# Kernel tuning notes

Measured on AMD Instinct MI355X. Metric: run time of the kernel, lower is better.

The kernel has to match this reference:

```python
import jax, jax.numpy as jnp
import numpy as np

B, L, D, NLAYERS, MAX_NODES, DEG = 32, 512, 768, 3, 128, 8


def _build_graph():
    rng = np.random.default_rng(0)
    per = rng.integers(-32, 33, size=B // 2)
    sizes = np.concatenate([96 + per, 96 - per]).astype(np.int64)  # sum = 96*B = 3072, each in [64,128]
    N = int(sizes.sum())
    offs = np.concatenate([[0], np.cumsum(sizes)])
    batch = np.repeat(np.arange(B), sizes).astype(np.int64)
    pad_idx = np.zeros((B, MAX_NODES), np.int64)
    pad_mask = np.zeros((B, MAX_NODES), bool)
    src, dst = [], []
    for b in range(B):
        n = int(sizes[b])
        pad_idx[b, :n] = np.arange(offs[b], offs[b] + n)
        pad_mask[b, :n] = True
        src.append(rng.integers(offs[b], offs[b] + n, n * DEG))
        dst.append(rng.integers(offs[b], offs[b] + n, n * DEG))
    return N, batch, pad_idx, pad_mask, np.concatenate(src), np.concatenate(dst)


def setup_inputs() -> dict:
    N, batch, pad_idx, pad_mask, esrc, edst = _build_graph()
    key = jax.random.key(0)
    ks = jax.random.split(key, 8)
    s = 1.0 / np.sqrt(D)
    return {
        "x": jax.random.normal(ks[0], (N, D), jnp.float32),
        "text": jax.random.normal(ks[1], (B, L, D), jnp.float32),
        "batch_ent1_d_mask": jnp.ones((B, 1), jnp.float32),
        "batch_ent1_g_mask": jnp.ones((B, 1), jnp.float32),
        "gnn_ws": jax.random.normal(ks[2], (NLAYERS, D, D), jnp.float32) * s,
        "gnn_wn": jax.random.normal(ks[3], (NLAYERS, D, D), jnp.float32) * s,
        "gnn_b": jnp.zeros((NLAYERS, D), jnp.float32),
        "atom_w": jax.random.normal(ks[4], (D, D), jnp.float32) * s,
        "atom_b": jnp.zeros((D,), jnp.float32),
        "rand_emb": jax.random.normal(ks[5], (1, D), jnp.float32),
        "batch": jnp.asarray(batch),
        "pad_idx": jnp.asarray(pad_idx),
        "pad_mask": jnp.asarray(pad_mask),
        "edge_src": jnp.asarray(esrc),
        "edge_dst": jnp.asarray(edst),
    }


def reference(x, text, batch_ent1_d_mask, batch_ent1_g_mask, gnn_ws, gnn_wn, gnn_b,
              atom_w, atom_b, rand_emb, batch, pad_idx, pad_mask, edge_src, edge_dst):
    N = x.shape[0]
    E = edge_src.shape[0]
    maskf = pad_mask.astype(x.dtype)            # [B, M]
    n_per = maskf.sum(axis=1)                   # [B] num real nodes per graph
    # edge-neighbor mean counts (constants w.r.t. x)
    cnt = jax.ops.segment_sum(jnp.ones((E,), x.dtype), edge_dst, num_segments=N)
    inv_cnt = 1.0 / jnp.maximum(cnt, 1.0)
    cms = []
    for i in range(NLAYERS):
        # MoleGraphConv stand-in: mean neighbor aggregation + self transform
        msg = jax.ops.segment_sum(x[edge_src], edge_dst, num_segments=N) * inv_cnt[:, None]
        x = jax.nn.relu(x @ gnn_ws[i] + msg @ gnn_wn[i] + gnn_b[i])
        # ragged gather into padded [B, M, D]
        xp = x[pad_idx] * maskf[..., None]
        # graph -> text cross attention (softmax over text tokens; no mask needed)
        g2t = jax.nn.softmax(jnp.einsum('bmd,bld->bml', xp, text), axis=-1)
        g2t_out = jnp.einsum('bml,bld->bmd', g2t, text)            # [B, M, D]
        # text -> graph cross attention (mask padded nodes)
        t2g_logits = jnp.einsum('bld,bmd->blm', text, xp)
        t2g_logits = jnp.where(pad_mask[:, None, :], t2g_logits, jnp.float32(-1e9))
        t2g = jax.nn.softmax(t2g_logits, axis=-1)
        t2g_out = jnp.einsum('blm,bmd->bld', t2g, xp)              # [B, L, D]
        # mean over concatenated rows [n_i + L] per graph (pool_type=2)
        pooled = ((g2t_out * maskf[..., None]).sum(axis=1) + t2g_out.sum(axis=1)) \
                 / (n_per + jnp.float32(L))[:, None]
        cms.append(pooled)
    out_cms = jnp.mean(jnp.stack(cms, axis=1), axis=1)              # mean over layers
    out_t = text[:, 0, :]
    # scatter-mean of final node features per graph
    gsum = jax.ops.segment_sum(x, batch, num_segments=B)
    gcnt = jax.ops.segment_sum(jnp.ones((N,), x.dtype), batch, num_segments=B)
    xg = gsum / jnp.maximum(gcnt, 1.0)[:, None]
    # dropout is a no-op in eval mode
    out_g = jnp.tanh(xg @ atom_w + atom_b)
    z = rand_emb[0]
    dg = batch_ent1_d_mask * batch_ent1_g_mask
    return jnp.concatenate([
        out_t * batch_ent1_d_mask + (1 - batch_ent1_d_mask) * z,
        out_g * batch_ent1_g_mask + (1 - batch_ent1_g_mask) * z,
        out_cms * dg + (1 - dg) * z,
    ], axis=-1)
```

## Files before the change

kernel.cpp:

```cpp
#include <hip/hip_runtime.h>

#define D 768
#define B 32
#define L 512
#define M 128
#define NNODES 3072
#define NEDGES 24576

using bf16x8 = __attribute__((ext_vector_type(8))) short;
using f32x4  = __attribute__((ext_vector_type(4))) float;

__device__ __forceinline__ float bf2f(unsigned short u) {
  union { unsigned int i; float f; } v; v.i = ((unsigned int)u) << 16; return v.f;
}
__device__ __forceinline__ unsigned short f2bf(float f) {
  union { float f; unsigned int i; } v; v.f = f;
  unsigned int x = v.i;
  return (unsigned short)((x + 0x7FFFu + ((x >> 16) & 1u)) >> 16);
}
__device__ __forceinline__ float ldf(const void* p, size_t i, int f32) {
  return f32 ? ((const float*)p)[i] : bf2f(((const unsigned short*)p)[i]);
}
__device__ __forceinline__ int ldi(const void* p, size_t i, int w64) {
  return w64 ? (int)((const long long*)p)[i] : ((const int*)p)[i];
}
__device__ __forceinline__ f32x4 mfma16(bf16x8 a, bf16x8 b, f32x4 c) {
  return __builtin_amdgcn_mfma_f32_16x16x32_bf16(a, b, c, 0, 0, 0);
}
__device__ __forceinline__ void gl_lds(const unsigned short* gsrc, unsigned short* lbase,
                                       int lane) {
  __builtin_amdgcn_global_load_lds(
      (const __attribute__((address_space(1))) unsigned int*)(gsrc + lane * 8),
      (__attribute__((address_space(3))) unsigned int*)lbase, 16, 0, 0);
}

__device__ __forceinline__ float pk_read(const unsigned short* P, int p, int l, int d) {
  return bf2f(P[(((size_t)(p * 24 + (d >> 5))) << 9) + ((((d & 31) >> 3) << 4) + l) * 8 + (d & 7)]);
}

__device__ __forceinline__ void fma8(float* acc, float w, uint4 v) {
  unsigned xs[4] = {v.x, v.y, v.z, v.w};
#pragma unroll
  for (int j = 0; j < 4; ++j) {
    acc[2 * j]     += w * bf2f((unsigned short)(xs[j] & 0xFFFFu));
    acc[2 * j + 1] += w * bf2f((unsigned short)(xs[j] >> 16));
  }
}

__device__ __forceinline__ void acc12(float* a, const uint2* u) {
#pragma unroll
  for (int j = 0; j < 3; ++j) {
    a[j * 4 + 0] += bf2f((unsigned short)(u[j].x & 0xFFFFu));
    a[j * 4 + 1] += bf2f((unsigned short)(u[j].x >> 16));
    a[j * 4 + 2] += bf2f((unsigned short)(u[j].y & 0xFFFFu));
    a[j * 4 + 3] += bf2f((unsigned short)(u[j].y >> 16));
  }
}


__device__ void d_pack_in(const void* src, unsigned short* rows, unsigned short* dst,
                          int p, int tid, int f) {
  unsigned short* pb = dst + (size_t)p * 12288;
  uint4 qv[6];
  if (f) {
    float4 v0[6], v1[6];
#pragma unroll
    for (int j = 0; j < 6; ++j) {
      int odx = j * 256 + tid;
      int kk = odx >> 6, lanep = odx & 63;
      size_t sbase = (size_t)(p * 16 + (lanep & 15)) * 768 + kk * 32 + ((lanep >> 4) << 3);
      const float* sp = (const float*)src + sbase;
      v0[j] = *(const float4*)sp;
      v1[j] = *(const float4*)(sp + 4);
    }
#pragma unroll
    for (int j = 0; j < 6; ++j) {
      union { unsigned short v[8]; uint4 q; } u;
      u.v[0] = f2bf(v0[j].x); u.v[1] = f2bf(v0[j].y); u.v[2] = f2bf(v0[j].z); u.v[3] = f2bf(v0[j].w);
      u.v[4] = f2bf(v1[j].x); u.v[5] = f2bf(v1[j].y); u.v[6] = f2bf(v1[j].z); u.v[7] = f2bf(v1[j].w);
      qv[j] = u.q;
    }
  } else {
#pragma unroll
    for (int j = 0; j < 6; ++j) {
      int odx = j * 256 + tid;
      int kk = odx >> 6, lanep = odx & 63;
      size_t sbase = (size_t)(p * 16 + (lanep & 15)) * 768 + kk * 32 + ((lanep >> 4) << 3);
      qv[j] = *(const uint4*)((const unsigned short*)src + sbase);
    }
  }
#pragma unroll
  for (int j = 0; j < 6; ++j) {
    int odx = j * 256 + tid;
    int kk = odx >> 6, lanep = odx & 63;
    size_t sbase = (size_t)(p * 16 + (lanep & 15)) * 768 + kk * 32 + ((lanep >> 4) << 3);
    if (rows) *(uint4*)&rows[sbase] = qv[j];
    *(uint4*)&pb[(size_t)odx * 8] = qv[j];
  }
}

__device__ void d_pack(const unsigned short* src, unsigned short* dst,
                       int p, int tid) {
  unsigned short* pb = dst + (size_t)p * 12288;
  uint4 qv[6];
#pragma unroll
  for (int j = 0; j < 6; ++j) {
    int odx = j * 256 + tid;
    int kk = odx >> 6, lanep = odx & 63;
    size_t sbase = (size_t)(p * 16 + (lanep & 15)) * 768 + kk * 32 + ((lanep >> 4) << 3);
    qv[j] = *(const uint4*)(src + sbase);
  }
#pragma unroll
  for (int j = 0; j < 6; ++j) {
    *(uint4*)&pb[(size_t)(j * 256 + tid) * 8] = qv[j];
  }
}

__device__ void d_wpack(const void* Ws, const void* Wn, const void* Aw, int f,
                        unsigned short* WsPk, unsigned short* WnPk, unsigned short* AwPk,
                        int r0, int tid) {
  int z = r0 / 288, rem = r0 % 288;
  int nblk = rem % 12, kk = rem / 12;
  const void* src; unsigned short* dst; size_t zoff;
  if (z < 3)      { src = Ws; zoff = (size_t)z * D * D;       dst = WsPk + zoff; }
  else if (z < 6) { src = Wn; zoff = (size_t)(z - 3) * D * D; dst = WnPk + zoff; }
  else            { src = Aw; zoff = 0;                       dst = AwPk; }
  int pl = tid >> 6, lane = tid & 63;
  int pG = nblk * 4 + pl;
  int k0 = kk * 32 + ((lane >> 4) << 3);
  int n  = nblk * 64 + pl * 16 + (lane & 15);
  union { unsigned short v[8]; uint4 q; } u;
  if (f) {
    const float* sp = (const float*)src + zoff + (size_t)k0 * D + n;
#pragma unroll
    for (int e = 0; e < 8; ++e) u.v[e] = f2bf(sp[(size_t)e * D]);
  } else {
    const unsigned short* sp = (const unsigned short*)src + zoff + (size_t)k0 * D + n;
#pragma unroll
    for (int e = 0; e < 8; ++e) u.v[e] = sp[(size_t)e * D];
  }
  *(uint4*)&dst[(((size_t)(pG * 24 + kk)) << 9) + lane * 8] = u.q;
}

__device__ void d_count(const void* edst, const void* batch, int w,
                        int* cnt, int* gcnt, int i) {
  if (i < NEDGES) atomicAdd(&cnt[ldi(edst, i, w)], 1);
  if (i < NNODES) atomicAdd(&gcnt[ldi(batch, i, w)], 1);
}

__device__ void d_msg(const unsigned short* x, const int* cnt, const int* rowstart,
                      const int* csr, unsigned short* Mpk, int p, int tid) {
  int w = tid >> 6, lane = tid & 63;
  unsigned short* pb = Mpk + (size_t)p * 12288;
#pragma unroll
  for (int i = 0; i < 4; i += 2) {
    int rA = w * 4 + i, rB = rA + 1;
    int nA = p * 16 + rA, nB = p * 16 + rB;
    int degA = cnt[nA], baseA = rowstart[nA];
    int degB = cnt[nB], baseB = rowstart[nB];
    float aA[12], aB[12];
#pragma unroll
    for (int j = 0; j < 12; ++j) { aA[j] = 0.f; aB[j] = 0.f; }
    int dmax = degA > degB ? degA : degB;
    for (int e = 0; e < dmax; ++e) {
      uint2 uA[3], uB[3];
      if (e < degA) {
        const uint2* xr = (const uint2*)(x + (size_t)csr[baseA + e] * D);
        uA[0] = xr[lane]; uA[1] = xr[lane + 64]; uA[2] = xr[lane + 128];
      }
      if (e < degB) {
        const uint2* xr = (const uint2*)(x + (size_t)csr[baseB + e] * D);
        uB[0] = xr[lane]; uB[1] = xr[lane + 64]; uB[2] = xr[lane + 128];
      }
      if (e < degA) acc12(aA, uA);
      if (e < degB) acc12(aB, uB);
    }
    float invA = 1.0f / (float)(degA > 1 ? degA : 1);
    float invB = 1.0f / (float)(degB > 1 ? degB : 1);
#pragma unroll
    for (int j = 0; j < 3; ++j) {
      int d0 = (lane + j * 64) * 4;
      int kk = d0 >> 5, q = (d0 >> 3) & 3, e0 = d0 & 7;
      uint2 wA, wB;
      wA.x = (unsigned int)f2bf(aA[j * 4 + 0] * invA)
           | ((unsigned int)f2bf(aA[j * 4 + 1] * invA) << 16);
      wA.y = (unsigned int)f2bf(aA[j * 4 + 2] * invA)
           | ((unsigned int)f2bf(aA[j * 4 + 3] * invA) << 16);
      wB.x = (unsigned int)f2bf(aB[j * 4 + 0] * invB)
           | ((unsigned int)f2bf(aB[j * 4 + 1] * invB) << 16);
      wB.y = (unsigned int)f2bf(aB[j * 4 + 2] * invB)
           | ((unsigned int)f2bf(aB[j * 4 + 3] * invB) << 16);
      *(uint2*)&pb[kk * 512 + (q * 16 + rA) * 8 + e0] = wA;
      *(uint2*)&pb[kk * 512 + (q * 16 + rB) * 8 + e0] = wB;
    }
  }
}

__device__ void d_gemm(const unsigned short* Xpk, const unsigned short* Mpk,
                       const unsigned short* WsPk, const unsigned short* WnPk,
                       const void* bias, size_t bias_off, int f,
                       unsigned short* Y, int bx, int by, int tid, char* smem) {
  unsigned short* lds = (unsigned short*)smem;
  int wave = tid >> 6, lane = tid & 63;
  int q = lane >> 4, t = lane & 15;
  int wm = wave >> 1, wn = wave & 1;
  int pa = bx * 4, pb = by * 4;
  f32x4 acc[2][2];
#pragma unroll
  for (int mi = 0; mi < 2; ++mi)
#pragma unroll
    for (int ni = 0; ni < 2; ++ni)
      acc[mi][ni] = (f32x4){0.f, 0.f, 0.f, 0.f};
  int c0 = wave * 2;
  int pan0 = (wave < 2) ? (pa + c0) : (pb + c0 - 4);
  auto issue = [&](int r) {
    unsigned short* dbuf = &lds[(r % 3) * 8192 + c0 * 512];
#pragma unroll
    for (int st = 0; st < 2; ++st) {
      int s = r * 2 + st;
      int h = (s >= 24) ? 1 : 0;
      const unsigned short* P = (wave < 2) ? (h ? Mpk : Xpk) : (h ? WnPk : WsPk);
      int kk = s - h * 24;
      gl_lds(P + (((size_t)(pan0 * 24 + kk)) << 9), dbuf + st * 4096, lane);
      gl_lds(P + (((size_t)((pan0 + 1) * 24 + kk)) << 9), dbuf + st * 4096 + 512, lane);
    }
  };
  issue(0);
  issue(1);
  for (int r = 0; r < 24; ++r) {
    if (r < 23) asm volatile("s_waitcnt vmcnt(4)" ::: "memory");
    else        asm volatile("s_waitcnt vmcnt(0)" ::: "memory");
    __builtin_amdgcn_s_barrier();
    asm volatile("" ::: "memory");
    if (r < 22) issue(r + 2);
    const unsigned short* bb = &lds[(r % 3) * 8192];
#pragma unroll
    for (int st = 0; st < 2; ++st) {
      const unsigned short* bs = bb + st * 4096;
      bf16x8 a0 = *(const bf16x8*)&bs[(wm * 2 + 0) * 512 + lane * 8];
      bf16x8 a1 = *(const bf16x8*)&bs[(wm * 2 + 1) * 512 + lane * 8];
      bf16x8 b0 = *(const bf16x8*)&bs[(4 + wn * 2 + 0) * 512 + lane * 8];
      bf16x8 b1 = *(const bf16x8*)&bs[(4 + wn * 2 + 1) * 512 + lane * 8];
      acc[0][0] = mfma16(a0, b0, acc[0][0]);
      acc[0][1] = mfma16(a0, b1, acc[0][1]);
      acc[1][0] = mfma16(a1, b0, acc[1][0]);
      acc[1][1] = mfma16(a1, b1, acc[1][1]);
    }
    asm volatile("" ::: "memory");
  }
#pragma unroll
  for (int ni = 0; ni < 2; ++ni) {
    int col = by * 64 + wn * 32 + ni * 16 + t;
    float bv = ldf(bias, bias_off + col, f);
#pragma unroll
    for (int mi = 0; mi < 2; ++mi) {
#pragma unroll
      for (int r = 0; r < 4; ++r) {
        int row = bx * 64 + wm * 32 + mi * 16 + q * 4 + r;
        float v = acc[mi][ni][r] + bv;
        Y[(size_t)row * D + col] = f2bf(v > 0.f ? v : 0.f);
      }
    }
  }
}

__device__ void d_xp(const unsigned short* Xn, const void* pidx, int w64,
                     const int* gcnt, unsigned short* xp, unsigned short* XpPk,
                     float* xgacc, int p, int tid, char* smem) {
  unsigned short* rows = (unsigned short*)smem;
  int r = tid >> 4, c16 = tid & 15;
  int bm = p * 16 + r;
  int b = bm >> 7, m = bm & 127;
  int nb = gcnt[b];
  uint4* dl = (uint4*)&rows[r * 776];
  uint4 v[6];
  if (m < nb) {
    const uint4* srcr = (const uint4*)(Xn + (size_t)ldi(pidx, bm, w64) * D);
#pragma unroll
    for (int j = 0; j < 6; ++j) v[j] = srcr[c16 + j * 16];
  } else {
    uint4 z = {0u, 0u, 0u, 0u};
#pragma unroll
    for (int j = 0; j < 6; ++j) v[j] = z;
  }
#pragma unroll
  for (int j = 0; j < 6; ++j) dl[c16 + j * 16] = v[j];
  __syncthreads();
#pragma unroll
  for (int j = 0; j < 6; ++j) {
    int idx = j * 256 + tid;
    int rr = idx / 96, cc = idx % 96;
    uint4 vv = *(const uint4*)&rows[rr * 776 + cc * 8];
    *(uint4*)&xp[(size_t)(p * 16 + rr) * D + cc * 8] = vv;
  }
  unsigned short* pb = XpPk + (size_t)p * 12288;
#pragma unroll
  for (int j = 0; j < 6; ++j) {
    int odx = j * 256 + tid;
    int kk = odx >> 6, lanep = odx & 63;
    int rr = lanep & 15, cg = lanep >> 4;
    int cc = kk * 4 + cg;
    uint4 vv = *(const uint4*)&rows[rr * 776 + cc * 8];
    *(uint4*)&pb[odx * 8] = vv;
  }
  if (xgacc) {
    int bb = p >> 3;
#pragma unroll
    for (int j = 0; j < 3; ++j) {
      int d = j * 256 + tid;
      float s = 0.f;
#pragma unroll
      for (int rr = 0; rr < 16; ++rr) s += bf2f(rows[rr * 776 + d]);
      atomicAdd(&xgacc[(size_t)bb * D + d], s);
    }
  }
}

__device__ void d_scores(const unsigned short* XpPk, const unsigned short* Tpk,
                         float* S, int bx, int by, int bz, int tid, char* smem) {
  unsigned short* lds = (unsigned short*)smem;
  int wave = tid >> 6, lane = tid & 63;
  int q = lane >> 4, t = lane & 15;
  int wm = wave >> 1, wn = wave & 1;
  int pa = bz * 8 + bx * 4;
  int pb = bz * 32 + by * 4;
  f32x4 acc[2][2];
#pragma unroll
  for (int mi = 0; mi < 2; ++mi)
#pragma unroll
    for (int ni = 0; ni < 2; ++ni)
      acc[mi][ni] = (f32x4){0.f, 0.f, 0.f, 0.f};
  int c0 = wave * 2;
  const unsigned short* P = (wave < 2) ? XpPk : Tpk;
  int pan0 = (wave < 2) ? (pa + c0) : (pb + c0 - 4);
  auto issue = [&](int r) {
    unsigned short* dbuf = &lds[(r % 3) * 8192 + c0 * 512];
#pragma unroll
    for (int st = 0; st < 2; ++st) {
      int kk = r * 2 + st;
      gl_lds(P + (((size_t)(pan0 * 24 + kk)) << 9), dbuf + st * 4096, lane);
      gl_lds(P + (((size_t)((pan0 + 1) * 24 + kk)) << 9), dbuf + st * 4096 + 512, lane);
    }
  };
  issue(0);
  issue(1);
  for (int r = 0; r < 12; ++r) {
    if (r < 11) asm volatile("s_waitcnt vmcnt(4)" ::: "memory");
    else        asm volatile("s_waitcnt vmcnt(0)" ::: "memory");
    __builtin_amdgcn_s_barrier();
    asm volatile("" ::: "memory");
    if (r < 10) issue(r + 2);
    const unsigned short* bb = &lds[(r % 3) * 8192];
#pragma unroll
    for (int st = 0; st < 2; ++st) {
      const unsigned short* bs = bb + st * 4096;
      bf16x8 a0 = *(const bf16x8*)&bs[(wm * 2 + 0) * 512 + lane * 8];
      bf16x8 a1 = *(const bf16x8*)&bs[(wm * 2 + 1) * 512 + lane * 8];
      bf16x8 b0 = *(const bf16x8*)&bs[(4 + wn * 2 + 0) * 512 + lane * 8];
      bf16x8 b1 = *(const bf16x8*)&bs[(4 + wn * 2 + 1) * 512 + lane * 8];
      acc[0][0] = mfma16(a0, b0, acc[0][0]);
      acc[0][1] = mfma16(a0, b1, acc[0][1]);
      acc[1][0] = mfma16(a1, b0, acc[1][0]);
      acc[1][1] = mfma16(a1, b1, acc[1][1]);
    }
    asm volatile("" ::: "memory");
  }
  float* Sb = S + (size_t)bz * M * L;
#pragma unroll
  for (int ni = 0; ni < 2; ++ni) {
    int col = by * 64 + wn * 32 + ni * 16 + t;
#pragma unroll
    for (int mi = 0; mi < 2; ++mi) {
#pragma unroll
      for (int r = 0; r < 4; ++r) {
        int row = bx * 64 + wm * 32 + mi * 16 + q * 4 + r;
        Sb[(size_t)row * L + col] = acc[mi][ni][r];
      }
    }
  }
}

__device__ void d_stats(const float* S, const int* gcnt, float* rmax, float* rsum,
                        float* cmaxv, float* csumv, int bid, int tid, char* smem) {
  if (bid < B * M) {
    float* red = (float*)smem;
    int lane = tid & 63, wv = tid >> 6;
    const float* r = S + (size_t)bid * L;
    float s0 = r[tid], s1 = r[tid + 256];
    float m = fmaxf(s0, s1);
#pragma unroll
    for (int o = 32; o > 0; o >>= 1) m = fmaxf(m, __shfl_down(m, o));
    if (lane == 0) red[wv] = m;
    __syncthreads();
    float bm = fmaxf(fmaxf(red[0], red[1]), fmaxf(red[2], red[3]));
    __syncthreads();
    float e = __expf(s0 - bm) + __expf(s1 - bm);
#pragma unroll
    for (int o = 32; o > 0; o >>= 1) e += __shfl_down(e, o);
    if (lane == 0) red[wv] = e;
    __syncthreads();
    if (tid == 0) { rmax[bid] = bm; rsum[bid] = red[0] + red[1] + red[2] + red[3]; }
  } else {
    float (*pm)[64] = (float(*)[64])smem;
    float (*ps)[64] = (float(*)[64])(smem + 1024);
    int cid = bid - B * M;
    int b = cid >> 3, ly = cid & 7;
    int w = tid >> 6, lane = tid & 63;
    int l = ly * 64 + lane;
    int nb = gcnt[b];
    const float* Sb = S + (size_t)b * M * L;
    int m0 = w * 32, m1 = min(m0 + 32, nb);
    float cm = -1e30f, cs = 0.f;
    for (int m = m0; m < m1; ++m) {
      float s = Sb[(size_t)m * L + l];
      if (s > cm) { cs = cs * __expf(cm - s) + 1.f; cm = s; }
      else cs += __expf(s - cm);
    }
    pm[w][lane] = cm; ps[w][lane] = cs;
    __syncthreads();
    if (w == 0) {
      float CM = -1e30f;
#pragma unroll
      for (int j = 0; j < 4; ++j) CM = fmaxf(CM, pm[j][lane]);
      float CS = 0.f;
#pragma unroll
      for (int j = 0; j < 4; ++j) CS += ps[j][lane] * __expf(pm[j][lane] - CM);
      cmaxv[b * L + l] = CM; csumv[b * L + l] = CS;
    }
  }
}

__device__ void d_cross(const float* S, const float* rmax, const float* rsum,
                        const float* cmaxv, const float* csumv, const int* gcnt,
                        float* wv, float* t2gcol, int bid, int tid, char* smem) {
  if (bid < 256) {
    float* rm = (float*)smem;
    float* ri = (float*)(smem + 512);
    float (*pw)[64] = (float(*)[64])(smem + 1024);
    int b = bid >> 3, ly = bid & 7;
    int w = tid >> 6, lane = tid & 63;
    if (tid < M) { rm[tid] = rmax[b * M + tid]; ri[tid] = 1.f / rsum[b * M + tid]; }
    __syncthreads();
    int l = ly * 64 + lane;
    int nb = gcnt[b];
    const float* Sb = S + (size_t)b * M * L;
    int m0 = w * 32, m1 = min(m0 + 32, nb);
    float wp = 0.f;
    for (int m = m0; m < m1; ++m)
      wp += __expf(Sb[(size_t)m * L + l] - rm[m]) * ri[m];
    pw[w][lane] = wp;
    __syncthreads();
    if (w == 0)
      wv[b * L + l] = pw[0][lane] + pw[1][lane] + pw[2][lane] + pw[3][lane];
  } else {
    float* red = (float*)smem;
    int bm = bid - 256;
    int b = bm >> 7, m = bm & 127;
    int lane = tid & 63, w = tid >> 6;
    int nb = gcnt[b];
    float acc = 0.f;
    if (m < nb) {
      const float* r = S + (size_t)bm * L;
      const float* cm = cmaxv + b * L;
      const float* cs = csumv + b * L;
      acc = __expf(r[tid] - cm[tid]) / cs[tid]
          + __expf(r[tid + 256] - cm[tid + 256]) / cs[tid + 256];
    }
#pragma unroll
    for (int o = 32; o > 0; o >>= 1) acc += __shfl_down(acc, o);
    if (lane == 0) red[w] = acc;
    __syncthreads();
    if (tid == 0) t2gcol[bm] = red[0] + red[1] + red[2] + red[3];
  }
}

__device__ void d_pooled(const float* wv, const float* t2gcol, const unsigned short* Tpk,
                         const unsigned short* xp, const int* gcnt, float* pooled,
                         int bid, int tid, char* smem) {
  float* lred = (float*)smem;
  float* wbuf = (float*)(smem + 3072);
  int b = bid / 10, seg = bid - b * 10;
  int chunk = tid % 96, half = tid / 96;
  int d = chunk * 8;
  float acc[8];
#pragma unroll
  for (int j = 0; j < 8; ++j) acc[j] = 0.f;
  if (tid < 64) {
    wbuf[tid] = (seg < 8) ? wv[b * L + seg * 64 + tid]
                          : t2gcol[b * M + (seg - 8) * 64 + tid];
  }
  __syncthreads();
  if (half < 2) {
    if (seg < 8) {
      int pbase = b * 32 + seg * 4;
      size_t cbase = ((size_t)(d >> 5)) << 9;
      int coff = ((d & 31) >> 3) << 4;
      for (int i = 0; i < 32; ++i) {
        int l = half * 32 + i;
        const unsigned short* src =
            Tpk + (((size_t)((pbase + (l >> 4)) * 24)) << 9) + cbase +
            (size_t)(coff + (l & 15)) * 8;
        fma8(acc, wbuf[l], *(const uint4*)src);
      }
    } else {
      const unsigned short* Xb = xp + (size_t)b * M * D + d;
      int m0 = (seg - 8) * 64;
      for (int i = 0; i < 32; ++i) {
        int mm = half * 32 + i;
        fma8(acc, wbuf[mm], *(const uint4*)&Xb[(size_t)(m0 + mm) * D]);
      }
    }
  }
  if (half == 1) {
#pragma unroll
    for (int j = 0; j < 8; ++j) lred[chunk * 8 + j] = acc[j];
  }
  __syncthreads();
  if (half == 0) {
    float inv = 1.f / ((float)gcnt[b] + 512.f);
#pragma unroll
    for (int j = 0; j < 8; ++j)
      atomicAdd(&pooled[(size_t)b * D + d + j], (acc[j] + lred[chunk * 8 + j]) * inv);
  }
}

__device__ void d_atom(const float* xgacc, const int* gcnt, const unsigned short* AwPk,
                       float* gpre, int bid, int tid) {
  int w = tid >> 6, lane = tid & 63;
  int q = lane >> 4, t = lane & 15;
  int nbase = bid * 64 + w * 16;
  int pb = nbase >> 4;
  int n0 = gcnt[t], n1 = gcnt[16 + t];
  float inv0 = 1.f / (float)(n0 > 1 ? n0 : 1);
  float inv1 = 1.f / (float)(n1 > 1 ? n1 : 1);
  f32x4 acc[2];
  acc[0] = (f32x4){0.f, 0.f, 0.f, 0.f};
  acc[1] = (f32x4){0.f, 0.f, 0.f, 0.f};
  for (int kk = 0; kk < 24; ++kk) {
    const float* s0 = xgacc + (size_t)t * D + kk * 32 + q * 8;
    const float* s1 = xgacc + (size_t)(16 + t) * D + kk * 32 + q * 8;
    union { unsigned short v[8]; bf16x8 f; } a0, a1;
#pragma unroll
    for (int j = 0; j < 8; ++j) { a0.v[j] = f2bf(s0[j] * inv0); a1.v[j] = f2bf(s1[j] * inv1); }
    bf16x8 bv = *(const bf16x8*)(AwPk + (((size_t)(pb * 24 + kk)) << 9) + (lane << 3));
    acc[0] = mfma16(a0.f, bv, acc[0]);
    acc[1] = mfma16(a1.f, bv, acc[1]);
  }
#pragma unroll
  for (int mi = 0; mi < 2; ++mi)
#pragma unroll
    for (int r = 0; r < 4; ++r) {
      int row = mi * 16 + q * 4 + r;
      gpre[(size_t)row * D + nbase + t] = acc[mi][r];
    }
}


__global__ void k_init(int* cnt, int* cursor, int* gcnt, float* pooled, float* xgacc,
                       const unsigned short* __restrict__ t,
                       const unsigned int* __restrict__ e, int* __restrict__ flags) {
  int i = blockIdx.x * 256 + threadIdx.x;
  if (i < NNODES) { cnt[i] = 0; cursor[i] = 0; }
  if (i < B) gcnt[i] = 0;
  if (i < B * D) { pooled[i] = 0.f; xgacc[i] = 0.f; }
  if (blockIdx.x == 0) {
    __shared__ int r0[256];
    __shared__ unsigned r1[256];
    int tid = threadIdx.x;
    int bad = 0;
    for (int j = tid; j < 8192; j += 256) {
      unsigned short u = t[2 * j];
      unsigned ex = (u >> 7) & 0xFF;
      if (ex >= 0xC0) bad = 1;
    }
    unsigned o = 0;
    for (int j = tid; j < NEDGES / 2; j += 256) o |= e[2 * j + 1];
    r0[tid] = bad; r1[tid] = o;
    __syncthreads();
    for (int s = 128; s > 0; s >>= 1) {
      if (tid < s) { r0[tid] |= r0[tid + s]; r1[tid] |= r1[tid + s]; }
      __syncthreads();
    }
    if (tid == 0) { flags[0] = r0[0]; flags[1] = (r1[0] == 0) ? 1 : 0; }
  }
}

__global__ __launch_bounds__(256) void k_setup2(
    const void* x_in, unsigned short* x0, unsigned short* PkA,
    const void* text, unsigned short* Tpk,
    const void* Ws, const void* Wn, const void* Aw,
    unsigned short* WsPk, unsigned short* WnPk, unsigned short* AwPk,
    const void* edst, const void* batch, int* cnt, int* gcnt,
    const int* __restrict__ flags) {
  int bid = blockIdx.x, tid = threadIdx.x;
  if (bid < 1216) {
    int f = flags[0];
    if (bid < NNODES / 16) d_pack_in(x_in, x0, PkA, bid, tid, f);
    else d_pack_in(text, nullptr, Tpk, bid - NNODES / 16, tid, f);
  } else if (bid < 3232) {
    d_wpack(Ws, Wn, Aw, flags[0], WsPk, WnPk, AwPk, bid - 1216, tid);
  } else {
    d_count(edst, batch, flags[1], cnt, gcnt, (bid - 3232) * 256 + tid);
  }
}

__global__ void k_scan(const int* __restrict__ cnt, int* __restrict__ rowstart) {
  __shared__ int a[NNODES], b[NNODES];
  int tid = threadIdx.x;
  for (int i = tid; i < NNODES; i += 1024) a[i] = cnt[i];
  __syncthreads();
  int* s = a; int* d = b;
  for (int off = 1; off < NNODES; off <<= 1) {
    for (int i = tid; i < NNODES; i += 1024)
      d[i] = s[i] + (i >= off ? s[i - off] : 0);
    __syncthreads();
    int* t = s; s = d; d = t;
  }
  for (int i = tid; i < NNODES; i += 1024) rowstart[i + 1] = s[i];
  if (tid == 0) rowstart[0] = 0;
}

__global__ void k_scatter(const void* __restrict__ esrc, const void* __restrict__ edst,
                          const int* __restrict__ flags, const int* __restrict__ rowstart,
                          int* __restrict__ cursor, int* __restrict__ csr) {
  int w = flags[1];
  int i = blockIdx.x * 256 + threadIdx.x;
  if (i < NEDGES) {
    int dd = ldi(edst, i, w);
    int pos = atomicAdd(&cursor[dd], 1);
    csr[rowstart[dd] + pos] = ldi(esrc, i, w);
  }
}

__global__ __launch_bounds__(256) void k_msgp(
    const unsigned short* x, const int* cnt, const int* rowstart, const int* csr,
    unsigned short* Mpk) {
  d_msg(x, cnt, rowstart, csr, Mpk, blockIdx.x, threadIdx.x);
}

__device__ __forceinline__ void gemm_map(int g, int& bx, int& by) {
  int gs = (g % 8) * 72 + g / 8;
  bx = gs / 12; by = gs % 12;
}
__device__ __forceinline__ void sc_map(int g, int& bx, int& by, int& bz) {
  int gs = (g % 8) * 64 + g / 8;
  bx = gs & 1; by = (gs >> 1) & 7; bz = gs >> 4;
}

__global__ __launch_bounds__(256) void k_gemm(
    const unsigned short* Apk, const unsigned short* Mpk,
    const unsigned short* WsPk, const unsigned short* WnPk,
    const void* bias, unsigned long bias_off, const int* flags, unsigned short* Y) {
  extern __shared__ char smem[];
  int bx, by; gemm_map(blockIdx.x, bx, by);
  d_gemm(Apk, Mpk, WsPk, WnPk, bias, bias_off, flags[0], Y, bx, by,
         threadIdx.x, smem);
}

__global__ __launch_bounds__(256) void k_postg(
    const unsigned short* Y, unsigned short* Npk, int packN,
    const void* pidx, const int* flags, const int* gcnt,
    unsigned short* xp, unsigned short* XpPk, float* xgacc) {
  extern __shared__ char smem[];
  int bid = blockIdx.x, tid = threadIdx.x;
  if (bid < 256) d_xp(Y, pidx, flags[1], gcnt, xp, XpPk, xgacc, bid, tid, smem);
  else d_pack(Y, Npk, bid - 256, tid);
}

__global__ __launch_bounds__(256) void k_scmsg(
    const unsigned short* XpPk, const unsigned short* Tpk, float* S,
    int msgN, const unsigned short* x, const int* cnt, const int* rowstart,
    const int* csr, unsigned short* Mpk) {
  extern __shared__ char smem[];
  int bid = blockIdx.x, tid = threadIdx.x;
  if (bid < msgN) d_msg(x, cnt, rowstart, csr, Mpk, bid, tid);
  else {
    int bx, by, bz; sc_map(bid - msgN, bx, by, bz);
    d_scores(XpPk, Tpk, S, bx, by, bz, tid, smem);
  }
}

__global__ __launch_bounds__(256) void k_stgemm(
    const float* S, const int* gcnt, float* rmax, float* rsum, float* cmaxv, float* csumv,
    int gemmN, const unsigned short* Apk, const unsigned short* Mpk,
    const unsigned short* WsPk, const unsigned short* WnPk,
    const void* bias, unsigned long bias_off, const int* flags, unsigned short* Y) {
  extern __shared__ char smem[];
  int bid = blockIdx.x, tid = threadIdx.x;
  if (bid < gemmN) {
    int bx, by; gemm_map(bid, bx, by);
    d_gemm(Apk, Mpk, WsPk, WnPk, bias, bias_off, flags[0], Y, bx, by, tid, smem);
  } else d_stats(S, gcnt, rmax, rsum, cmaxv, csumv, bid - gemmN, tid, smem);
}

__global__ __launch_bounds__(256) void k_crpostg(
    const float* S, const float* rmax, const float* rsum, const float* cmaxv,
    const float* csumv, const int* gcnt, float* wv, float* t2gcol,
    int packN, int xpN, const unsigned short* Y, unsigned short* Npk,
    const void* pidx, const int* flags, unsigned short* xp, unsigned short* XpPk,
    float* xgacc) {
  extern __shared__ char smem[];
  int bid = blockIdx.x, tid = threadIdx.x;
  if (bid < packN) { d_pack(Y, Npk, bid, tid); return; }
  int r = bid - packN;
  if (r < xpN) { d_xp(Y, pidx, flags[1], gcnt, xp, XpPk, xgacc, r, tid, smem); return; }
  d_cross(S, rmax, rsum, cmaxv, csumv, gcnt, wv, t2gcol, r - xpN, tid, smem);
}

__global__ __launch_bounds__(256) void k_plscmsg(
    const float* wv, const float* t2gcol, const unsigned short* Tpk,
    const unsigned short* xpL, const int* gcnt, float* pooled,
    int scN, const unsigned short* XpPk, float* S,
    int msgN, const unsigned short* x, const int* cnt, const int* rowstart,
    const int* csr, unsigned short* Mpk,
    int atomN, const float* xgacc, const unsigned short* AwPk, float* gpre) {
  extern __shared__ char smem[];
  int bid = blockIdx.x, tid = threadIdx.x;
  if (bid < msgN) { d_msg(x, cnt, rowstart, csr, Mpk, bid, tid); return; }
  int r = bid - msgN;
  if (r < scN) {
    int bx, by, bz; sc_map(r, bx, by, bz);
    d_scores(XpPk, Tpk, S, bx, by, bz, tid, smem); return;
  }
  r -= scN;
  if (r < 320) { d_pooled(wv, t2gcol, Tpk, xpL, gcnt, pooled, r, tid, smem); return; }
  d_atom(xgacc, gcnt, AwPk, gpre, r - 320, tid);
}

__global__ __launch_bounds__(256) void k_final(
    const unsigned short* __restrict__ Tpk, const float* __restrict__ gpre,
    const float* __restrict__ pooled, const void* __restrict__ ab,
    const void* __restrict__ dmask, const void* __restrict__ gmask,
    const void* __restrict__ remb, const int* __restrict__ flags,
    void* __restrict__ out) {
  int f = flags[0];
  int b = blockIdx.x, tid = threadIdx.x;
  float dm = ldf(dmask, b, f);
  float gm = ldf(gmask, b, f);
  float dg = dm * gm;
  size_t base = (size_t)b * 2304;
#pragma unroll
  for (int j = 0; j < 3; ++j) {
    int d = tid + j * 256;
    float z = ldf(remb, d, f);
    float tv = pk_read(Tpk, b * 32, 0, d);
    float o0 = tv * dm + (1.f - dm) * z;
    float gv = tanhf(gpre[(size_t)b * D + d] + ldf(ab, d, f));
    float o1 = gv * gm + (1.f - gm) * z;
    float p = pooled[(size_t)b * D + d] * (1.f / 3.f);
    float o2 = p * dg + (1.f - dg) * z;
    if (f) {
      float* of = (float*)out;
      of[base + d] = o0; of[base + 768 + d] = o1; of[base + 1536 + d] = o2;
    } else {
      unsigned short* ob = (unsigned short*)out;
      ob[base + d] = f2bf(o0); ob[base + 768 + d] = f2bf(o1); ob[base + 1536 + d] = f2bf(o2);
    }
  }
}

extern "C" void kernel_launch(void* const* d_in, const int* in_sizes, int n_in,
                              void* d_out, int out_size, void* d_ws, size_t ws_size,
                              hipStream_t stream) {
  const void* x_in  = d_in[0];
  const void* text  = d_in[1];
  const void* dmask = d_in[2];
  const void* gmask = d_in[3];
  const void* gws   = d_in[4];
  const void* gwn   = d_in[5];
  const void* gb    = d_in[6];
  const void* aw    = d_in[7];
  const void* ab    = d_in[8];
  const void* remb  = d_in[9];
  const void* batch = d_in[10];
  const void* pidx  = d_in[11];
  const void* esrc  = d_in[13];
  const void* edst  = d_in[14];

  char* wsp = (char*)d_ws;
  size_t off = 0;
  auto carve = [&](size_t bytes) -> void* {
    void* p = wsp + off;
    off += (bytes + 255) & ~(size_t)255;
    return p;
  };
  int* flags = (int*)carve(2 * 4);
  unsigned short* x0    = (unsigned short*)carve((size_t)NNODES * D * 2);
  unsigned short* xA    = (unsigned short*)carve((size_t)NNODES * D * 2);
  unsigned short* xB    = (unsigned short*)carve((size_t)NNODES * D * 2);
  unsigned short* PkA   = (unsigned short*)carve((size_t)NNODES * D * 2);
  unsigned short* PkB   = (unsigned short*)carve((size_t)NNODES * D * 2);
  unsigned short* Mpk   = (unsigned short*)carve((size_t)NNODES * D * 2);
  unsigned short* Tpk   = (unsigned short*)carve((size_t)B * L * D * 2);
  unsigned short* WsPk  = (unsigned short*)carve((size_t)3 * D * D * 2);
  unsigned short* WnPk  = (unsigned short*)carve((size_t)3 * D * D * 2);
  unsigned short* AwPk  = (unsigned short*)carve((size_t)D * D * 2);
  unsigned short* xpA   = (unsigned short*)carve((size_t)B * M * D * 2);
  unsigned short* xpB   = (unsigned short*)carve((size_t)B * M * D * 2);
  unsigned short* XpPkA = (unsigned short*)carve((size_t)B * M * D * 2);
  unsigned short* XpPkB = (unsigned short*)carve((size_t)B * M * D * 2);
  float* xgacc   = (float*)carve((size_t)B * D * 4);
  float* gpre    = (float*)carve((size_t)B * D * 4);
  float* S       = (float*)carve((size_t)B * M * L * 4);
  float* rmax    = (float*)carve((size_t)B * M * 4);
  float* rsum    = (float*)carve((size_t)B * M * 4);
  float* wv      = (float*)carve((size_t)B * L * 4);
  float* cmaxv   = (float*)carve((size_t)B * L * 4);
  float* csumv   = (float*)carve((size_t)B * L * 4);
  float* t2gcol  = (float*)carve((size_t)B * M * 4);
  float* pooled  = (float*)carve((size_t)B * D * 4);
  int* cnt      = (int*)carve((size_t)NNODES * 4);
  int* rowstart = (int*)carve((size_t)(NNODES + 1) * 4);
  int* cursor   = (int*)carve((size_t)NNODES * 4);
  int* gcnt     = (int*)carve((size_t)B * 4);
  int* csr      = (int*)carve((size_t)NEDGES * 4);

  const size_t DD = (size_t)D * D;

  k_init<<<96, 256, 0, stream>>>(cnt, cursor, gcnt, pooled, xgacc,
                                 (const unsigned short*)text, (const unsigned int*)edst, flags);
  k_setup2<<<3328, 256, 0, stream>>>(x_in, x0, PkA, text, Tpk, gws, gwn, aw,
                                     WsPk, WnPk, AwPk, edst, batch, cnt, gcnt, flags);
  k_scan<<<1, 1024, 0, stream>>>(cnt, rowstart);
  k_scatter<<<96, 256, 0, stream>>>(esrc, edst, flags, rowstart, cursor, csr);

  k_msgp<<<192, 256, 0, stream>>>(x0, cnt, rowstart, csr, Mpk);
  k_gemm<<<576, 256, 49152, stream>>>(PkA, Mpk, WsPk, WnPk, gb, 0, flags, xA);
  k_postg<<<448, 256, 24832, stream>>>(xA, PkB, 192, pidx, flags, gcnt, xpA, XpPkA, nullptr);
  k_scmsg<<<704, 256, 49152, stream>>>(XpPkA, Tpk, S, 192, xA, cnt, rowstart, csr, Mpk);
  k_stgemm<<<4928, 256, 49152, stream>>>(S, gcnt, rmax, rsum, cmaxv, csumv,
                                         576, PkB, Mpk, WsPk + DD, WnPk + DD, gb, D, flags, xB);
  k_crpostg<<<4800, 256, 24832, stream>>>(S, rmax, rsum, cmaxv, csumv, gcnt, wv, t2gcol,
                                          192, 256, xB, PkA, pidx, flags, xpB, XpPkB, nullptr);
  k_plscmsg<<<1024, 256, 49152, stream>>>(wv, t2gcol, Tpk, xpA, gcnt, pooled,
                                          512, XpPkB, S, 192, xB, cnt, rowstart, csr, Mpk,
                                          0, nullptr, nullptr, nullptr);
  k_stgemm<<<4928, 256, 49152, stream>>>(S, gcnt, rmax, rsum, cmaxv, csumv,
                                         576, PkA, Mpk, WsPk + 2 * DD, WnPk + 2 * DD,
                                         gb, 2 * D, flags, xA);
  k_crpostg<<<4608, 256, 24832, stream>>>(S, rmax, rsum, cmaxv, csumv, gcnt, wv, t2gcol,
                                          0, 256, xA, nullptr, pidx, flags, xpA, XpPkA, xgacc);
  k_plscmsg<<<832, 256, 49152, stream>>>(wv, t2gcol, Tpk, xpB, gcnt, pooled,
                                         512, XpPkA, S, 0, nullptr, nullptr, nullptr,
                                         nullptr, nullptr, 0, nullptr, nullptr, nullptr);
  k_stgemm<<<4352, 256, 2048, stream>>>(S, gcnt, rmax, rsum, cmaxv, csumv,
                                        0, nullptr, nullptr, nullptr, nullptr,
                                        nullptr, 0, flags, nullptr);
  k_crpostg<<<4352, 256, 2048, stream>>>(S, rmax, rsum, cmaxv, csumv, gcnt, wv, t2gcol,
                                         0, 0, nullptr, nullptr, pidx, flags,
                                         nullptr, nullptr, nullptr);
  k_plscmsg<<<332, 256, 4096, stream>>>(wv, t2gcol, Tpk, xpA, gcnt, pooled,
                                        0, nullptr, nullptr, 0, nullptr, nullptr, nullptr,
                                        nullptr, nullptr, 12, xgacc, AwPk, gpre);
  k_final<<<32, 256, 0, stream>>>(Tpk, gpre, pooled, ab, dmask, gmask, remb, flags, d_out);
}
```

Before: 434.0 us.

## Deepen GEMM LDS pipeline, shrink LDS, reorder fused block roles, aggregate gcnt atomics

The GEMM and scores mainloops switch from three 2-step LDS stages to a four-slot ring of single k-steps, three of them in flight, which shrinks LDS per block from 48KB to 32KB so more blocks can be resident. The fused kernels reorder block-index dispatch so the long stats/cross/pooled/scores work is placed in the low block indices and the short pack/msg work in the high ones. The node-count atomics are aggregated per wave through a ballot run-length, and the pack routines interleave load and store instead of batching loads. The risk is less latency hiding per barrier, since each barrier now covers half as much MFMA work.

```diff
diff --git a/kernel.cpp b/kernel.cpp
--- a/kernel.cpp
+++ b/kernel.cpp
@@ -61,58 +61,39 @@
 __device__ void d_pack_in(const void* src, unsigned short* rows, unsigned short* dst,
                           int p, int tid, int f) {
   unsigned short* pb = dst + (size_t)p * 12288;
-  uint4 qv[6];
-  if (f) {
-    float4 v0[6], v1[6];
-#pragma unroll
-    for (int j = 0; j < 6; ++j) {
-      int odx = j * 256 + tid;
-      int kk = odx >> 6, lanep = odx & 63;
-      size_t sbase = (size_t)(p * 16 + (lanep & 15)) * 768 + kk * 32 + ((lanep >> 4) << 3);
-      const float* sp = (const float*)src + sbase;
-      v0[j] = *(const float4*)sp;
-      v1[j] = *(const float4*)(sp + 4);
-    }
-#pragma unroll
-    for (int j = 0; j < 6; ++j) {
-      union { unsigned short v[8]; uint4 q; } u;
-      u.v[0] = f2bf(v0[j].x); u.v[1] = f2bf(v0[j].y); u.v[2] = f2bf(v0[j].z); u.v[3] = f2bf(v0[j].w);
-      u.v[4] = f2bf(v1[j].x); u.v[5] = f2bf(v1[j].y); u.v[6] = f2bf(v1[j].z); u.v[7] = f2bf(v1[j].w);
-      qv[j] = u.q;
-    }
-  } else {
-#pragma unroll
-    for (int j = 0; j < 6; ++j) {
-      int odx = j * 256 + tid;
-      int kk = odx >> 6, lanep = odx & 63;
-      size_t sbase = (size_t)(p * 16 + (lanep & 15)) * 768 + kk * 32 + ((lanep >> 4) << 3);
-      qv[j] = *(const uint4*)((const unsigned short*)src + sbase);
-    }
-  }
 #pragma unroll
   for (int j = 0; j < 6; ++j) {
     int odx = j * 256 + tid;
     int kk = odx >> 6, lanep = odx & 63;
-    size_t sbase = (size_t)(p * 16 + (lanep & 15)) * 768 + kk * 32 + ((lanep >> 4) << 3);
-    if (rows) *(uint4*)&rows[sbase] = qv[j];
-    *(uint4*)&pb[(size_t)odx * 8] = qv[j];
+    int q = lanep >> 4, r16 = lanep & 15;
+    int row = p * 16 + r16, col0 = kk * 32 + q * 8;
+    size_t sbase = (size_t)row * 768 + col0;
+    union { unsigned short v[8]; uint4 qv; } u;
+    if (f) {
+      const float* sp = (const float*)src + sbase;
+      float4 v0 = *(const float4*)sp;
+      float4 v1 = *(const float4*)(sp + 4);
+      u.v[0] = f2bf(v0.x); u.v[1] = f2bf(v0.y); u.v[2] = f2bf(v0.z); u.v[3] = f2bf(v0.w);
+      u.v[4] = f2bf(v1.x); u.v[5] = f2bf(v1.y); u.v[6] = f2bf(v1.z); u.v[7] = f2bf(v1.w);
+    } else {
+      u.qv = *(const uint4*)((const unsigned short*)src + sbase);
+    }
+    if (rows) *(uint4*)&rows[sbase] = u.qv;
+    *(uint4*)&pb[(size_t)odx * 8] = u.qv;
   }
 }
 
 __device__ void d_pack(const unsigned short* src, unsigned short* dst,
                        int p, int tid) {
   unsigned short* pb = dst + (size_t)p * 12288;
-  uint4 qv[6];
 #pragma unroll
   for (int j = 0; j < 6; ++j) {
     int odx = j * 256 + tid;
     int kk = odx >> 6, lanep = odx & 63;
-    size_t sbase = (size_t)(p * 16 + (lanep & 15)) * 768 + kk * 32 + ((lanep >> 4) << 3);
-    qv[j] = *(const uint4*)(src + sbase);
-  }
-#pragma unroll
-  for (int j = 0; j < 6; ++j) {
-    *(uint4*)&pb[(size_t)(j * 256 + tid) * 8] = qv[j];
+    int q = lanep >> 4, r16 = lanep & 15;
+    size_t sbase = (size_t)(p * 16 + r16) * 768 + kk * 32 + q * 8;
+    uint4 qv = *(const uint4*)(src + sbase);
+    *(uint4*)&pb[(size_t)odx * 8] = qv;
   }
 }
 
@@ -145,7 +126,18 @@
 __device__ void d_count(const void* edst, const void* batch, int w,
                         int* cnt, int* gcnt, int i) {
   if (i < NEDGES) atomicAdd(&cnt[ldi(edst, i, w)], 1);
-  if (i < NNODES) atomicAdd(&gcnt[ldi(batch, i, w)], 1);
+  if (i < NNODES) {
+    int b = ldi(batch, i, w);
+    int lane = i & 63;
+    int prev = __shfl_up(b, 1);
+    bool first = (lane == 0) || (prev != b);
+    unsigned long long bm = __ballot(first ? 1 : 0);
+    if (first) {
+      unsigned long long higher = (lane < 63) ? (bm >> (lane + 1)) : 0ULL;
+      int next = higher ? (lane + __ffsll((long long)higher)) : 64;
+      atomicAdd(&gcnt[b], next - lane);
+    }
+  }
 }
 
 __device__ void d_msg(const unsigned short* x, const int* cnt, const int* rowstart,
@@ -213,39 +205,31 @@
       acc[mi][ni] = (f32x4){0.f, 0.f, 0.f, 0.f};
   int c0 = wave * 2;
   int pan0 = (wave < 2) ? (pa + c0) : (pb + c0 - 4);
-  auto issue = [&](int r) {
-    unsigned short* dbuf = &lds[(r % 3) * 8192 + c0 * 512];
-#pragma unroll
-    for (int st = 0; st < 2; ++st) {
-      int s = r * 2 + st;
-      int h = (s >= 24) ? 1 : 0;
-      const unsigned short* P = (wave < 2) ? (h ? Mpk : Xpk) : (h ? WnPk : WsPk);
-      int kk = s - h * 24;
-      gl_lds(P + (((size_t)(pan0 * 24 + kk)) << 9), dbuf + st * 4096, lane);
-      gl_lds(P + (((size_t)((pan0 + 1) * 24 + kk)) << 9), dbuf + st * 4096 + 512, lane);
-    }
+  auto issue = [&](int s) {
+    int h = (s >= 24) ? 1 : 0;
+    const unsigned short* P = (wave < 2) ? (h ? Mpk : Xpk) : (h ? WnPk : WsPk);
+    int kk = s - h * 24;
+    unsigned short* dbuf = &lds[(s & 3) * 4096 + c0 * 512];
+    gl_lds(P + (((size_t)(pan0 * 24 + kk)) << 9), dbuf, lane);
+    gl_lds(P + (((size_t)((pan0 + 1) * 24 + kk)) << 9), dbuf + 512, lane);
   };
-  issue(0);
-  issue(1);
-  for (int r = 0; r < 24; ++r) {
-    if (r < 23) asm volatile("s_waitcnt vmcnt(4)" ::: "memory");
-    else        asm volatile("s_waitcnt vmcnt(0)" ::: "memory");
+  issue(0); issue(1); issue(2);
+  for (int r = 0; r < 48; ++r) {
+    if (r < 46)       asm volatile("s_waitcnt vmcnt(4)" ::: "memory");
+    else if (r == 46) asm volatile("s_waitcnt vmcnt(2)" ::: "memory");
+    else              asm volatile("s_waitcnt vmcnt(0)" ::: "memory");
     __builtin_amdgcn_s_barrier();
     asm volatile("" ::: "memory");
-    if (r < 22) issue(r + 2);
-    const unsigned short* bb = &lds[(r % 3) * 8192];
-#pragma unroll
-    for (int st = 0; st < 2; ++st) {
-      const unsigned short* bs = bb + st * 4096;
-      bf16x8 a0 = *(const bf16x8*)&bs[(wm * 2 + 0) * 512 + lane * 8];
-      bf16x8 a1 = *(const bf16x8*)&bs[(wm * 2 + 1) * 512 + lane * 8];
-      bf16x8 b0 = *(const bf16x8*)&bs[(4 + wn * 2 + 0) * 512 + lane * 8];
-      bf16x8 b1 = *(const bf16x8*)&bs[(4 + wn * 2 + 1) * 512 + lane * 8];
-      acc[0][0] = mfma16(a0, b0, acc[0][0]);
-      acc[0][1] = mfma16(a0, b1, acc[0][1]);
-      acc[1][0] = mfma16(a1, b0, acc[1][0]);
-      acc[1][1] = mfma16(a1, b1, acc[1][1]);
-    }
+    if (r + 3 < 48) issue(r + 3);
+    const unsigned short* bs = &lds[(r & 3) * 4096];
+    bf16x8 a0 = *(const bf16x8*)&bs[(wm * 2 + 0) * 512 + lane * 8];
+    bf16x8 a1 = *(const bf16x8*)&bs[(wm * 2 + 1) * 512 + lane * 8];
+    bf16x8 b0 = *(const bf16x8*)&bs[(4 + wn * 2 + 0) * 512 + lane * 8];
+    bf16x8 b1 = *(const bf16x8*)&bs[(4 + wn * 2 + 1) * 512 + lane * 8];
+    acc[0][0] = mfma16(a0, b0, acc[0][0]);
+    acc[0][1] = mfma16(a0, b1, acc[0][1]);
+    acc[1][0] = mfma16(a1, b0, acc[1][0]);
+    acc[1][1] = mfma16(a1, b1, acc[1][1]);
     asm volatile("" ::: "memory");
   }
 #pragma unroll
@@ -333,36 +317,28 @@
   int c0 = wave * 2;
   const unsigned short* P = (wave < 2) ? XpPk : Tpk;
   int pan0 = (wave < 2) ? (pa + c0) : (pb + c0 - 4);
-  auto issue = [&](int r) {
-    unsigned short* dbuf = &lds[(r % 3) * 8192 + c0 * 512];
-#pragma unroll
-    for (int st = 0; st < 2; ++st) {
-      int kk = r * 2 + st;
-      gl_lds(P + (((size_t)(pan0 * 24 + kk)) << 9), dbuf + st * 4096, lane);
-      gl_lds(P + (((size_t)((pan0 + 1) * 24 + kk)) << 9), dbuf + st * 4096 + 512, lane);
-    }
+  auto issue = [&](int kk) {
+    unsigned short* dbuf = &lds[(kk & 3) * 4096 + c0 * 512];
+    gl_lds(P + (((size_t)(pan0 * 24 + kk)) << 9), dbuf, lane);
+    gl_lds(P + (((size_t)((pan0 + 1) * 24 + kk)) << 9), dbuf + 512, lane);
   };
-  issue(0);
-  issue(1);
-  for (int r = 0; r < 12; ++r) {
-    if (r < 11) asm volatile("s_waitcnt vmcnt(4)" ::: "memory");
-    else        asm volatile("s_waitcnt vmcnt(0)" ::: "memory");
+  issue(0); issue(1); issue(2);
+  for (int r = 0; r < 24; ++r) {
+    if (r < 22)       asm volatile("s_waitcnt vmcnt(4)" ::: "memory");
+    else if (r == 22) asm volatile("s_waitcnt vmcnt(2)" ::: "memory");
+    else              asm volatile("s_waitcnt vmcnt(0)" ::: "memory");
     __builtin_amdgcn_s_barrier();
     asm volatile("" ::: "memory");
-    if (r < 10) issue(r + 2);
-    const unsigned short* bb = &lds[(r % 3) * 8192];
-#pragma unroll
-    for (int st = 0; st < 2; ++st) {
-      const unsigned short* bs = bb + st * 4096;
-      bf16x8 a0 = *(const bf16x8*)&bs[(wm * 2 + 0) * 512 + lane * 8];
-      bf16x8 a1 = *(const bf16x8*)&bs[(wm * 2 + 1) * 512 + lane * 8];
-      bf16x8 b0 = *(const bf16x8*)&bs[(4 + wn * 2 + 0) * 512 + lane * 8];
-      bf16x8 b1 = *(const bf16x8*)&bs[(4 + wn * 2 + 1) * 512 + lane * 8];
-      acc[0][0] = mfma16(a0, b0, acc[0][0]);
-      acc[0][1] = mfma16(a0, b1, acc[0][1]);
-      acc[1][0] = mfma16(a1, b0, acc[1][0]);
-      acc[1][1] = mfma16(a1, b1, acc[1][1]);
-    }
+    if (r + 3 < 24) issue(r + 3);
+    const unsigned short* bs = &lds[(r & 3) * 4096];
+    bf16x8 a0 = *(const bf16x8*)&bs[(wm * 2 + 0) * 512 + lane * 8];
+    bf16x8 a1 = *(const bf16x8*)&bs[(wm * 2 + 1) * 512 + lane * 8];
+    bf16x8 b0 = *(const bf16x8*)&bs[(4 + wn * 2 + 0) * 512 + lane * 8];
+    bf16x8 b1 = *(const bf16x8*)&bs[(4 + wn * 2 + 1) * 512 + lane * 8];
+    acc[0][0] = mfma16(a0, b0, acc[0][0]);
+    acc[0][1] = mfma16(a0, b1, acc[0][1]);
+    acc[1][0] = mfma16(a1, b0, acc[1][0]);
+    acc[1][1] = mfma16(a1, b1, acc[1][1]);
     asm volatile("" ::: "memory");
   }
   float* Sb = S + (size_t)bz * M * L;
@@ -663,8 +639,8 @@
     unsigned short* xp, unsigned short* XpPk, float* xgacc) {
   extern __shared__ char smem[];
   int bid = blockIdx.x, tid = threadIdx.x;
-  if (bid < 256) d_xp(Y, pidx, flags[1], gcnt, xp, XpPk, xgacc, bid, tid, smem);
-  else d_pack(Y, Npk, bid - 256, tid);
+  if (bid < packN) d_pack(Y, Npk, bid, tid);
+  else d_xp(Y, pidx, flags[1], gcnt, xp, XpPk, xgacc, bid - packN, tid, smem);
 }
 
 __global__ __launch_bounds__(256) void k_scmsg(
@@ -673,11 +649,10 @@
     const int* csr, unsigned short* Mpk) {
   extern __shared__ char smem[];
   int bid = blockIdx.x, tid = threadIdx.x;
-  if (bid < msgN) d_msg(x, cnt, rowstart, csr, Mpk, bid, tid);
-  else {
-    int bx, by, bz; sc_map(bid - msgN, bx, by, bz);
+  if (bid < 512) {
+    int bx, by, bz; sc_map(bid, bx, by, bz);
     d_scores(XpPk, Tpk, S, bx, by, bz, tid, smem);
-  }
+  } else d_msg(x, cnt, rowstart, csr, Mpk, bid - 512, tid);
 }
 
 __global__ __launch_bounds__(256) void k_stgemm(
@@ -687,10 +662,11 @@
     const void* bias, unsigned long bias_off, const int* flags, unsigned short* Y) {
   extern __shared__ char smem[];
   int bid = blockIdx.x, tid = threadIdx.x;
-  if (bid < gemmN) {
-    int bx, by; gemm_map(bid, bx, by);
+  if (bid < 4352) d_stats(S, gcnt, rmax, rsum, cmaxv, csumv, bid, tid, smem);
+  else {
+    int bx, by; gemm_map(bid - 4352, bx, by);
     d_gemm(Apk, Mpk, WsPk, WnPk, bias, bias_off, flags[0], Y, bx, by, tid, smem);
-  } else d_stats(S, gcnt, rmax, rsum, cmaxv, csumv, bid - gemmN, tid, smem);
+  }
 }
 
 __global__ __launch_bounds__(256) void k_crpostg(
@@ -701,10 +677,12 @@
     float* xgacc) {
   extern __shared__ char smem[];
   int bid = blockIdx.x, tid = threadIdx.x;
-  if (bid < packN) { d_pack(Y, Npk, bid, tid); return; }
-  int r = bid - packN;
-  if (r < xpN) { d_xp(Y, pidx, flags[1], gcnt, xp, XpPk, xgacc, r, tid, smem); return; }
-  d_cross(S, rmax, rsum, cmaxv, csumv, gcnt, wv, t2gcol, r - xpN, tid, smem);
+  if (bid < 4352) d_cross(S, rmax, rsum, cmaxv, csumv, gcnt, wv, t2gcol, bid, tid, smem);
+  else {
+    int r = bid - 4352;
+    if (r < packN) d_pack(Y, Npk, r, tid);
+    else d_xp(Y, pidx, flags[1], gcnt, xp, XpPk, xgacc, r - packN, tid, smem);
+  }
 }
 
 __global__ __launch_bounds__(256) void k_plscmsg(
@@ -716,15 +694,15 @@
     int atomN, const float* xgacc, const unsigned short* AwPk, float* gpre) {
   extern __shared__ char smem[];
   int bid = blockIdx.x, tid = threadIdx.x;
-  if (bid < msgN) { d_msg(x, cnt, rowstart, csr, Mpk, bid, tid); return; }
-  int r = bid - msgN;
+  if (bid < 320) { d_pooled(wv, t2gcol, Tpk, xpL, gcnt, pooled, bid, tid, smem); return; }
+  int r = bid - 320;
   if (r < scN) {
     int bx, by, bz; sc_map(r, bx, by, bz);
     d_scores(XpPk, Tpk, S, bx, by, bz, tid, smem); return;
   }
   r -= scN;
-  if (r < 320) { d_pooled(wv, t2gcol, Tpk, xpL, gcnt, pooled, r, tid, smem); return; }
-  d_atom(xgacc, gcnt, AwPk, gpre, r - 320, tid);
+  if (r < msgN) { d_msg(x, cnt, rowstart, csr, Mpk, r, tid); return; }
+  d_atom(xgacc, gcnt, AwPk, gpre, r - msgN, tid);
 }
 
 __global__ __launch_bounds__(256) void k_final(
@@ -825,22 +803,22 @@
   k_scatter<<<96, 256, 0, stream>>>(esrc, edst, flags, rowstart, cursor, csr);
 
   k_msgp<<<192, 256, 0, stream>>>(x0, cnt, rowstart, csr, Mpk);
-  k_gemm<<<576, 256, 49152, stream>>>(PkA, Mpk, WsPk, WnPk, gb, 0, flags, xA);
+  k_gemm<<<576, 256, 32768, stream>>>(PkA, Mpk, WsPk, WnPk, gb, 0, flags, xA);
   k_postg<<<448, 256, 24832, stream>>>(xA, PkB, 192, pidx, flags, gcnt, xpA, XpPkA, nullptr);
-  k_scmsg<<<704, 256, 49152, stream>>>(XpPkA, Tpk, S, 192, xA, cnt, rowstart, csr, Mpk);
-  k_stgemm<<<4928, 256, 49152, stream>>>(S, gcnt, rmax, rsum, cmaxv, csumv,
+  k_scmsg<<<704, 256, 32768, stream>>>(XpPkA, Tpk, S, 192, xA, cnt, rowstart, csr, Mpk);
+  k_stgemm<<<4928, 256, 32768, stream>>>(S, gcnt, rmax, rsum, cmaxv, csumv,
                                          576, PkB, Mpk, WsPk + DD, WnPk + DD, gb, D, flags, xB);
   k_crpostg<<<4800, 256, 24832, stream>>>(S, rmax, rsum, cmaxv, csumv, gcnt, wv, t2gcol,
                                           192, 256, xB, PkA, pidx, flags, xpB, XpPkB, nullptr);
-  k_plscmsg<<<1024, 256, 49152, stream>>>(wv, t2gcol, Tpk, xpA, gcnt, pooled,
+  k_plscmsg<<<1024, 256, 32768, stream>>>(wv, t2gcol, Tpk, xpA, gcnt, pooled,
                                           512, XpPkB, S, 192, xB, cnt, rowstart, csr, Mpk,
                                           0, nullptr, nullptr, nullptr);
-  k_stgemm<<<4928, 256, 49152, stream>>>(S, gcnt, rmax, rsum, cmaxv, csumv,
+  k_stgemm<<<4928, 256, 32768, stream>>>(S, gcnt, rmax, rsum, cmaxv, csumv,
                                          576, PkA, Mpk, WsPk + 2 * DD, WnPk + 2 * DD,
                                          gb, 2 * D, flags, xA);
   k_crpostg<<<4608, 256, 24832, stream>>>(S, rmax, rsum, cmaxv, csumv, gcnt, wv, t2gcol,
                                           0, 256, xA, nullptr, pidx, flags, xpA, XpPkA, xgacc);
-  k_plscmsg<<<832, 256, 49152, stream>>>(wv, t2gcol, Tpk, xpB, gcnt, pooled,
+  k_plscmsg<<<832, 256, 32768, stream>>>(wv, t2gcol, Tpk, xpB, gcnt, pooled,
                                          512, XpPkA, S, 0, nullptr, nullptr, nullptr,
                                          nullptr, nullptr, 0, nullptr, nullptr, nullptr);
   k_stgemm<<<4352, 256, 2048, stream>>>(S, gcnt, rmax, rsum, cmaxv, csumv,
```

Result: slower. 463.0 us (+6.7%).
